# Kernel optimization log

Hardware: AMD Instinct MI355X
Metric: run time of the kernel (lower is better)

## Reference

```python
import jax, jax.numpy as jnp
import numpy as np

BATCH = 4096
IN_DIM = 2048      # pooled CNN feature dim
OUT_DIM = 14951    # landmark classes
EPS = 1e-12        # tf.nn.l2_normalize epsilon


def _hadamard_slice(rows, cols):
    # Sylvester Hadamard entry: H[i, j] = (-1)^popcount(i & j).
    # Builds only the [rows, cols] slice of the 16384x16384 matrix.
    i = jnp.arange(rows, dtype=jnp.uint32)[:, None]
    j = jnp.arange(cols, dtype=jnp.uint32)[None, :]
    par = jax.lax.population_count(i & j) & 1
    return 1.0 - 2.0 * par.astype(jnp.float32)


def setup_inputs() -> dict:
    key = jax.random.key(0)
    k1, k2 = jax.random.split(key)
    x = jax.random.normal(k1, (BATCH, IN_DIM), dtype=jnp.float32)
    init_scale = 1.0 / np.sqrt(OUT_DIM)
    scale = jnp.full((1,), init_scale, dtype=jnp.float32)
    bias = jax.random.uniform(k2, (OUT_DIM,), dtype=jnp.float32,
                              minval=-init_scale, maxval=init_scale)
    return {"x": x, "scale": scale, "bias": bias}


def reference(x, scale, bias):
    H = _hadamard_slice(x.shape[1], bias.shape[0])  # [IN_DIM, OUT_DIM], +-1
    # L2-normalize along last axis (matches K.l2_normalize / tf.nn.l2_normalize)
    xn = x * jax.lax.rsqrt(jnp.maximum(jnp.sum(x * x, axis=-1, keepdims=True), EPS))
    out = -scale * jnp.matmul(xn, H) + bias  # activation=None
    return out
```

## Files before the change

kernel.cpp:

```cpp
#include <hip/hip_runtime.h>

#define BATCH   4096
#define IN_DIM  2048
#define OUT_DIM 14951
#define NTHREADS 256

__global__ __launch_bounds__(NTHREADS) void HadamardClassifier_44487271252814_kernel(
    const float* __restrict__ x,
    const float* __restrict__ scale,
    const float* __restrict__ bias,
    float* __restrict__ out)
{
    __shared__ float y[IN_DIM];
    __shared__ float wsum[NTHREADS / 64];

    const int tid = threadIdx.x;
    const int b   = blockIdx.x;
    const float* xrow = x + (size_t)b * IN_DIM;

    float4 v0 = reinterpret_cast<const float4*>(xrow)[2 * tid];
    float4 v1 = reinterpret_cast<const float4*>(xrow)[2 * tid + 1];

    float ss = v0.x * v0.x + v0.y * v0.y + v0.z * v0.z + v0.w * v0.w
             + v1.x * v1.x + v1.y * v1.y + v1.z * v1.z + v1.w * v1.w;
    #pragma unroll
    for (int o = 32; o > 0; o >>= 1) ss += __shfl_down(ss, o, 64);
    if ((tid & 63) == 0) wsum[tid >> 6] = ss;

    float a0 = v0.x, a1 = v0.y, a2 = v0.z, a3 = v0.w;
    float a4 = v1.x, a5 = v1.y, a6 = v1.z, a7 = v1.w;
    float b0 = a0 + a1, b1 = a0 - a1, b2 = a2 + a3, b3 = a2 - a3;
    float b4 = a4 + a5, b5 = a4 - a5, b6 = a6 + a7, b7 = a6 - a7;
    float c0 = b0 + b2, c1 = b1 + b3, c2 = b0 - b2, c3 = b1 - b3;
    float c4 = b4 + b6, c5 = b5 + b7, c6 = b4 - b6, c7 = b5 - b7;
    a0 = c0 + c4; a1 = c1 + c5; a2 = c2 + c6; a3 = c3 + c7;
    a4 = c0 - c4; a5 = c1 - c5; a6 = c2 - c6; a7 = c3 - c7;

    const int base = 8 * tid;
    y[base + 0] = a0; y[base + 1] = a1; y[base + 2] = a2; y[base + 3] = a3;
    y[base + 4] = a4; y[base + 5] = a5; y[base + 6] = a6; y[base + 7] = a7;
    __syncthreads();

    #pragma unroll
    for (int h = 8; h < IN_DIM; h <<= 1) {
        #pragma unroll
        for (int r = 0; r < IN_DIM / 2 / NTHREADS; ++r) {
            int idx = tid + r * NTHREADS;
            int i = ((idx & ~(h - 1)) << 1) | (idx & (h - 1));
            float u = y[i];
            float w = y[i + h];
            y[i]     = u + w;
            y[i + h] = u - w;
        }
        __syncthreads();
    }

    float total = wsum[0] + wsum[1] + wsum[2] + wsum[3];
    float inv = rsqrtf(fmaxf(total, 1e-12f));
    float s = -scale[0] * inv;

    float* orow = out + (size_t)b * OUT_DIM;
    for (int j = tid; j < OUT_DIM; j += NTHREADS) {
        orow[j] = s * y[j & (IN_DIM - 1)] + bias[j];
    }
}

extern "C" void kernel_launch(void* const* d_in, const int* in_sizes, int n_in,
                              void* d_out, int out_size, void* d_ws, size_t ws_size,
                              hipStream_t stream) {
    const float* x     = (const float*)d_in[0];
    const float* scale = (const float*)d_in[1];
    const float* bias  = (const float*)d_in[2];
    float* out = (float*)d_out;

    hipLaunchKernelGGL(HadamardClassifier_44487271252814_kernel,
                       dim3(BATCH), dim3(NTHREADS), 0, stream,
                       x, scale, bias, out);
}
```

Before: 297.8 us.

## Process four rows per block with float4 FWHT stages and vectorized output stores

Each block now handles four batch rows with 512 threads. Each thread does a 16-point in-register butterfly, and the remaining shared-memory FWHT stages operate on float4 pairs. Output is written as a flat float4 stream across the four contiguous rows. This allows 16-byte stores to global memory despite the odd row length, and it cuts per-element butterfly instruction and sync overhead. In exchange, shared memory use per block rises, and the output loop gains row/column index arithmetic plus unaligned bias reads.

```diff
diff --git a/kernel.cpp b/kernel.cpp
--- a/kernel.cpp
+++ b/kernel.cpp
@@ -3,65 +3,111 @@
 #define BATCH   4096
 #define IN_DIM  2048
 #define OUT_DIM 14951
-#define NTHREADS 256
+#define ROWS    4
+#define NT      512
+#define STRIDE  2052
+#define EPS     1e-12f
 
-__global__ __launch_bounds__(NTHREADS) void HadamardClassifier_44487271252814_kernel(
+__global__ __launch_bounds__(NT, 8) void HadamardClassifier_44487271252814_kernel(
     const float* __restrict__ x,
     const float* __restrict__ scale,
     const float* __restrict__ bias,
     float* __restrict__ out)
 {
-    __shared__ float y[IN_DIM];
-    __shared__ float wsum[NTHREADS / 64];
+    __shared__ float y[ROWS * STRIDE];
+    __shared__ float rss[ROWS * 2];
+    __shared__ float srow[ROWS];
 
     const int tid = threadIdx.x;
-    const int b   = blockIdx.x;
-    const float* xrow = x + (size_t)b * IN_DIM;
+    const int r   = tid >> 7;
+    const int t   = tid & 127;
+    const int b0  = blockIdx.x * ROWS;
 
-    float4 v0 = reinterpret_cast<const float4*>(xrow)[2 * tid];
-    float4 v1 = reinterpret_cast<const float4*>(xrow)[2 * tid + 1];
+    const float4* xv = reinterpret_cast<const float4*>(x + (size_t)(b0 + r) * IN_DIM) + 4 * t;
+    float4 v0 = xv[0], v1 = xv[1], v2 = xv[2], v3 = xv[3];
+    float a[16] = { v0.x, v0.y, v0.z, v0.w, v1.x, v1.y, v1.z, v1.w,
+                    v2.x, v2.y, v2.z, v2.w, v3.x, v3.y, v3.z, v3.w };
 
-    float ss = v0.x * v0.x + v0.y * v0.y + v0.z * v0.z + v0.w * v0.w
-             + v1.x * v1.x + v1.y * v1.y + v1.z * v1.z + v1.w * v1.w;
+    float ss = 0.f;
+    #pragma unroll
+    for (int k = 0; k < 16; ++k) ss += a[k] * a[k];
     #pragma unroll
     for (int o = 32; o > 0; o >>= 1) ss += __shfl_down(ss, o, 64);
-    if ((tid & 63) == 0) wsum[tid >> 6] = ss;
+    if ((tid & 63) == 0) rss[tid >> 6] = ss;
 
-    float a0 = v0.x, a1 = v0.y, a2 = v0.z, a3 = v0.w;
-    float a4 = v1.x, a5 = v1.y, a6 = v1.z, a7 = v1.w;
-    float b0 = a0 + a1, b1 = a0 - a1, b2 = a2 + a3, b3 = a2 - a3;
-    float b4 = a4 + a5, b5 = a4 - a5, b6 = a6 + a7, b7 = a6 - a7;
-    float c0 = b0 + b2, c1 = b1 + b3, c2 = b0 - b2, c3 = b1 - b3;
-    float c4 = b4 + b6, c5 = b5 + b7, c6 = b4 - b6, c7 = b5 - b7;
-    a0 = c0 + c4; a1 = c1 + c5; a2 = c2 + c6; a3 = c3 + c7;
-    a4 = c0 - c4; a5 = c1 - c5; a6 = c2 - c6; a7 = c3 - c7;
+    #pragma unroll
+    for (int h = 1; h < 16; h <<= 1) {
+        #pragma unroll
+        for (int g = 0; g < 16; g += 2 * h) {
+            #pragma unroll
+            for (int k = 0; k < h; ++k) {
+                float u = a[g + k], w = a[g + k + h];
+                a[g + k]     = u + w;
+                a[g + k + h] = u - w;
+            }
+        }
+    }
 
-    const int base = 8 * tid;
-    y[base + 0] = a0; y[base + 1] = a1; y[base + 2] = a2; y[base + 3] = a3;
-    y[base + 4] = a4; y[base + 5] = a5; y[base + 6] = a6; y[base + 7] = a7;
+    float* yr = y + r * STRIDE;
+    #pragma unroll
+    for (int k = 0; k < 4; ++k) {
+        *reinterpret_cast<float4*>(&yr[16 * t + 4 * k]) =
+            make_float4(a[4 * k], a[4 * k + 1], a[4 * k + 2], a[4 * k + 3]);
+    }
     __syncthreads();
 
+    if (tid < ROWS)
+        srow[tid] = -scale[0] * rsqrtf(fmaxf(rss[2 * tid] + rss[2 * tid + 1], EPS));
+
     #pragma unroll
-    for (int h = 8; h < IN_DIM; h <<= 1) {
+    for (int h = 16; h < IN_DIM; h <<= 1) {
         #pragma unroll
-        for (int r = 0; r < IN_DIM / 2 / NTHREADS; ++r) {
-            int idx = tid + r * NTHREADS;
+        for (int q = 0; q < 2; ++q) {
+            int idx = 4 * (t + 128 * q);
             int i = ((idx & ~(h - 1)) << 1) | (idx & (h - 1));
-            float u = y[i];
-            float w = y[i + h];
-            y[i]     = u + w;
-            y[i + h] = u - w;
+            float4 u = *reinterpret_cast<float4*>(&yr[i]);
+            float4 w = *reinterpret_cast<float4*>(&yr[i + h]);
+            float4 su, sw;
+            su.x = u.x + w.x; su.y = u.y + w.y; su.z = u.z + w.z; su.w = u.w + w.w;
+            sw.x = u.x - w.x; sw.y = u.y - w.y; sw.z = u.z - w.z; sw.w = u.w - w.w;
+            *reinterpret_cast<float4*>(&yr[i])     = su;
+            *reinterpret_cast<float4*>(&yr[i + h]) = sw;
         }
         __syncthreads();
     }
 
-    float total = wsum[0] + wsum[1] + wsum[2] + wsum[3];
-    float inv = rsqrtf(fmaxf(total, 1e-12f));
-    float s = -scale[0] * inv;
+    float4* obase = reinterpret_cast<float4*>(out + (size_t)b0 * OUT_DIM);
+    const int NF4 = (ROWS * OUT_DIM) / 4;
 
-    float* orow = out + (size_t)b * OUT_DIM;
-    for (int j = tid; j < OUT_DIM; j += NTHREADS) {
-        orow[j] = s * y[j & (IN_DIM - 1)] + bias[j];
+    for (int f4 = tid; f4 < NF4; f4 += NT) {
+        int e  = f4 << 2;
+        int rr = (e >= OUT_DIM) + (e >= 2 * OUT_DIM) + (e >= 3 * OUT_DIM);
+        int j  = e - rr * OUT_DIM;
+        float4 o;
+        if (j + 3 < OUT_DIM) {
+            float sv = srow[rr];
+            const float* yq = y + rr * STRIDE;
+            int m = j & (IN_DIM - 1);
+            float y0 = yq[m];
+            float y1 = yq[(m + 1) & (IN_DIM - 1)];
+            float y2 = yq[(m + 2) & (IN_DIM - 1)];
+            float y3 = yq[(m + 3) & (IN_DIM - 1)];
+            o.x = fmaf(sv, y0, bias[j]);
+            o.y = fmaf(sv, y1, bias[j + 1]);
+            o.z = fmaf(sv, y2, bias[j + 2]);
+            o.w = fmaf(sv, y3, bias[j + 3]);
+        } else {
+            float tmp[4];
+            #pragma unroll
+            for (int c = 0; c < 4; ++c) {
+                int ee = e + c;
+                int rc = (ee >= OUT_DIM) + (ee >= 2 * OUT_DIM) + (ee >= 3 * OUT_DIM);
+                int jc = ee - rc * OUT_DIM;
+                tmp[c] = fmaf(srow[rc], y[rc * STRIDE + (jc & (IN_DIM - 1))], bias[jc]);
+            }
+            o = make_float4(tmp[0], tmp[1], tmp[2], tmp[3]);
+        }
+        obase[f4] = o;
     }
 }
 
@@ -74,6 +120,6 @@
     float* out = (float*)d_out;
 
     hipLaunchKernelGGL(HadamardClassifier_44487271252814_kernel,
-                       dim3(BATCH), dim3(NTHREADS), 0, stream,
+                       dim3(BATCH / ROWS), dim3(NT), 0, stream,
                        x, scale, bias, out);
 }
```

Result: faster. 288.4 us (-3.1%).
